# Kernel tuning notes

Measured on AMD Instinct MI355X. Metric: run time of the kernel, lower is better.

## Reference

```python
import jax, jax.numpy as jnp
import numpy as np

N = 8192
IN_F = 256
OUT_F = 64
ALPHA = 0.3  # LeakyReLU negative slope
NEG_INF = -9e15


def setup_inputs() -> dict:
    key = jax.random.key(0)
    k1, k2, k3, k4 = jax.random.split(key, 4)
    h = jax.random.normal(k1, (N, IN_F), dtype=jnp.float32)
    # sparse-ish binary adjacency with self loops (values are 0/1 floats)
    adj = (jax.random.uniform(k2, (N, N)) < 0.05).astype(jnp.float32)
    adj = jnp.maximum(adj, jnp.eye(N, dtype=jnp.float32))
    # xavier_uniform-style scales (gain=1.414)
    w_lim = 1.414 * np.sqrt(6.0 / (IN_F + OUT_F))
    a_lim = 1.414 * np.sqrt(6.0 / (2 * OUT_F + 1))
    W = jax.random.uniform(k3, (IN_F, OUT_F), minval=-w_lim, maxval=w_lim, dtype=jnp.float32)
    a = jax.random.uniform(k4, (2 * OUT_F, 1), minval=-a_lim, maxval=a_lim, dtype=jnp.float32)
    return {"h": h, "adj": adj, "W": W, "a": a}


def reference(h, adj, W, a):
    # Wh: [N, F]
    Wh = h @ W
    # Additive decomposition of the original concat-attention:
    # e_ij = leakyrelu(a[:F].Wh_i + a[F:].Wh_j)  -- identical math, no NxNx2F tensor
    src = Wh @ a[:OUT_F]      # [N, 1]
    dst = Wh @ a[OUT_F:]      # [N, 1]
    e = jax.nn.leaky_relu(src + dst.T, negative_slope=ALPHA)  # [N, N]
    e = e * adj               # faithful: original multiplies by adj before masking
    att = jnp.where(adj > 0, e, NEG_INF)
    att = jax.nn.softmax(att, axis=1)
    # dropout omitted (eval mode / deterministic reference)
    h_prime = att @ Wh        # [N, F]
    return jax.nn.elu(h_prime)
```

## Files before the change

kernel.cpp:

```cpp
#include <hip/hip_runtime.h>
#include <hip/hip_bf16.h>

#define N_NODES 8192
#define IN_F    256
#define OUT_F   64
#define ALPHA   0.3f
#define MBIAS   20.0f
#define CSPL    8
#define COLS_PER (N_NODES / CSPL)
#define NTILES  (COLS_PER / 64)
#define LDP     72
#define MROW    136
#define WH_BLOCKS (N_NODES / 16)

typedef unsigned short u16;
typedef unsigned int   u32;
typedef unsigned long long u64;
typedef __attribute__((ext_vector_type(8))) short bf16x8;
typedef __attribute__((ext_vector_type(4))) float f32x4;

__device__ __forceinline__ float bf2f(u32 u) { return __uint_as_float(u << 16); }
__device__ __forceinline__ u32 f2bfbits(float x) {
    u32 u = __float_as_uint(x);
    return (u + 0x7FFFu + ((u >> 16) & 1u)) >> 16;
}
__device__ __forceinline__ float lrelu(float s) { return s > 0.f ? s : ALPHA * s; }

__device__ __forceinline__ int detect_bf16(const void* adj) {
    return ((((const u32*)adj)[0] & 0xFFFFu) == 0x3F80u) ? 1 : 0;
}

template <bool BF16>
__device__ __forceinline__ float ld(const void* p, size_t idx) {
    if constexpr (BF16) return bf2f(((const u16*)p)[idx]);
    else                return ((const float*)p)[idx];
}

template <bool BF16>
__device__ __forceinline__ void wh4_impl(
    const void* __restrict__ h, const void* __restrict__ W,
    const void* __restrict__ a, float* __restrict__ src,
    float* __restrict__ dst, int i0, int lane, float* accv)
{
    float acc0 = 0.f, acc1 = 0.f, acc2 = 0.f, acc3 = 0.f;
#pragma unroll 8
    for (int k = 0; k < IN_F; ++k) {
        float wv = ld<BF16>(W, (size_t)k * OUT_F + lane);
        float h0 = ld<BF16>(h, (size_t)(i0 + 0) * IN_F + k);
        float h1 = ld<BF16>(h, (size_t)(i0 + 1) * IN_F + k);
        float h2 = ld<BF16>(h, (size_t)(i0 + 2) * IN_F + k);
        float h3 = ld<BF16>(h, (size_t)(i0 + 3) * IN_F + k);
        acc0 = fmaf(h0, wv, acc0);
        acc1 = fmaf(h1, wv, acc1);
        acc2 = fmaf(h2, wv, acc2);
        acc3 = fmaf(h3, wv, acc3);
    }
    float av = ld<BF16>(a, lane);
    float bv = ld<BF16>(a, OUT_F + lane);
    float accs[4] = {acc0, acc1, acc2, acc3};
#pragma unroll
    for (int r = 0; r < 4; ++r) {
        float ps = accs[r] * av, pd = accs[r] * bv;
#pragma unroll
        for (int off = 32; off > 0; off >>= 1) {
            ps += __shfl_xor(ps, off, 64);
            pd += __shfl_xor(pd, off, 64);
        }
        if (lane == 0) { src[i0 + r] = ps; dst[i0 + r] = pd; }
        accv[r] = accs[r];
    }
}

__global__ __launch_bounds__(256) void gat_prep_kernel(
    const void* __restrict__ h, const void* __restrict__ W,
    const void* __restrict__ a, const void* __restrict__ adj,
    u16* __restrict__ WhT, float* __restrict__ src, float* __restrict__ dst,
    u64* __restrict__ mask64)
{
    __shared__ float accs[16][OUT_F];
    const int tid = threadIdx.x, wave = tid >> 6, lane = tid & 63;
    const int isbf = detect_bf16(adj);

    if (blockIdx.x < WH_BLOCKS) {
        const int i0 = blockIdx.x * 16 + wave * 4;
        float av[4];
        if (isbf) wh4_impl<true >(h, W, a, src, dst, i0, lane, av);
        else      wh4_impl<false>(h, W, a, src, dst, i0, lane, av);
#pragma unroll
        for (int r = 0; r < 4; ++r) accs[wave * 4 + r][lane] = av[r];
        __syncthreads();
        if (tid < OUT_F) {
            u32 w[8];
#pragma unroll
            for (int e = 0; e < 8; ++e) {
                u32 lo = f2bfbits(accs[2 * e][tid]);
                u32 hi = f2bfbits(accs[2 * e + 1][tid]);
                w[e] = lo | (hi << 16);
            }
            u16* dstp = WhT + (size_t)tid * N_NODES + blockIdx.x * 16;
            *(uint4*)dstp       = *(uint4*)&w[0];
            *(uint4*)(dstp + 8) = *(uint4*)&w[4];
        }
    } else {
        const int wgid = (blockIdx.x - WH_BLOCKS) * 4 + wave;
        const int NW   = 2048 * 4;
        const int C    = (N_NODES / 256) * N_NODES;
        if (isbf) {
            const u16* base = (const u16*)adj;
            for (int c = wgid; c < C; c += NW) {
                const u16* p = base + (size_t)c * 256;
                u64 b0 = __ballot(p[lane]       != 0);
                u64 b1 = __ballot(p[64  + lane] != 0);
                u64 b2 = __ballot(p[128 + lane] != 0);
                u64 b3 = __ballot(p[192 + lane] != 0);
                u64 v = (lane == 0) ? b0 : (lane == 1) ? b1 : (lane == 2) ? b2 : b3;
                if (lane < 4) mask64[(size_t)c * 4 + lane] = v;
            }
        } else {
            const float* base = (const float*)adj;
            for (int c = wgid; c < C; c += NW) {
                const float* p = base + (size_t)c * 256;
                u64 b0 = __ballot(p[lane]       != 0.f);
                u64 b1 = __ballot(p[64  + lane] != 0.f);
                u64 b2 = __ballot(p[128 + lane] != 0.f);
                u64 b3 = __ballot(p[192 + lane] != 0.f);
                u64 v = (lane == 0) ? b0 : (lane == 1) ? b1 : (lane == 2) ? b2 : b3;
                if (lane < 4) mask64[(size_t)c * 4 + lane] = v;
            }
        }
    }
}

__global__ __launch_bounds__(256, 4) void gat_attn_kernel(
    const u64* __restrict__ mask64, const u16* __restrict__ WhT,
    const float* __restrict__ src, const float* __restrict__ dst,
    float* __restrict__ O_part, float* __restrict__ l_part)
{
    __shared__ alignas(16) u16 Plds[64 * LDP];
    __shared__ alignas(16) u16 Blds[64 * LDP];
    __shared__ alignas(16) unsigned char Mlds[64 * MROW];

    const int tid = threadIdx.x, wave = tid >> 6, lane = tid & 63;
    const int r = tid >> 2, cq = tid & 3;
    const int i0 = blockIdx.x * 64, c0 = blockIdx.y * COLS_PER;

    {
        const unsigned char* g = (const unsigned char*)mask64
            + (size_t)(i0 + r) * (N_NODES / 8) + (c0 >> 3) + cq * 32;
        *(uint4*)&Mlds[r * MROW + cq * 32]      = *(const uint4*)g;
        *(uint4*)&Mlds[r * MROW + cq * 32 + 16] = *(const uint4*)(g + 16);
    }

    const float srow = src[i0 + r];
    const float m = lrelu(srow + MBIAS);

    const u16*    whtrow = WhT + (size_t)r * N_NODES + c0 + cq * 16;
    const float4* dstp   = (const float4*)(dst + c0 + cq * 16);

    const int mrow = lane & 15, kq = (lane >> 4) * 8;

    f32x4 acc[4] = {{0,0,0,0},{0,0,0,0},{0,0,0,0},{0,0,0,0}};
    float lacc = 0.f;

    uint4 pb0 = *(const uint4*)(whtrow);
    uint4 pb1 = *(const uint4*)(whtrow + 8);

    __syncthreads();
    const u16* mrowp = (const u16*)&Mlds[r * MROW];

    for (int t = 0; t < NTILES; ++t) {
        *(uint4*)&Blds[r * LDP + cq * 16]     = pb0;
        *(uint4*)&Blds[r * LDP + cq * 16 + 8] = pb1;

        u32 msk = mrowp[t * 4 + cq];
        float4 d0 = dstp[t * 16],     d1 = dstp[t * 16 + 1];
        float4 d2 = dstp[t * 16 + 2], d3 = dstp[t * 16 + 3];
        float dv[16] = {d0.x,d0.y,d0.z,d0.w, d1.x,d1.y,d1.z,d1.w,
                        d2.x,d2.y,d2.z,d2.w, d3.x,d3.y,d3.z,d3.w};
        u32 po[8];
#pragma unroll
        for (int e = 0; e < 8; ++e) {
            float s0 = lrelu(srow + dv[2 * e]);
            float s1 = lrelu(srow + dv[2 * e + 1]);
            float p0 = (msk & (1u << (2 * e)))     ? __expf(s0 - m) : 0.f;
            float p1 = (msk & (1u << (2 * e + 1))) ? __expf(s1 - m) : 0.f;
            u32 q0 = f2bfbits(p0), q1 = f2bfbits(p1);
            lacc += bf2f(q0) + bf2f(q1);
            po[e] = q0 | (q1 << 16);
        }
        *(uint4*)&Plds[r * LDP + cq * 16]     = *(uint4*)&po[0];
        *(uint4*)&Plds[r * LDP + cq * 16 + 8] = *(uint4*)&po[4];

        __syncthreads();

        if (t + 1 < NTILES) {
            pb0 = *(const uint4*)(whtrow + (t + 1) * 64);
            pb1 = *(const uint4*)(whtrow + (t + 1) * 64 + 8);
        }

#pragma unroll
        for (int ks = 0; ks < 2; ++ks) {
            bf16x8 avf = *(bf16x8*)&Plds[(16 * wave + mrow) * LDP + ks * 32 + kq];
#pragma unroll
            for (int nt = 0; nt < 4; ++nt) {
                bf16x8 bvf = *(bf16x8*)&Blds[(16 * nt + mrow) * LDP + ks * 32 + kq];
                acc[nt] = __builtin_amdgcn_mfma_f32_16x16x32_bf16(avf, bvf, acc[nt], 0, 0, 0);
            }
        }
        __syncthreads();
    }

    lacc += __shfl_xor(lacc, 1, 64);
    lacc += __shfl_xor(lacc, 2, 64);
    if (cq == 0) l_part[blockIdx.y * N_NODES + i0 + r] = lacc;

    float* Ob = O_part + (size_t)blockIdx.y * N_NODES * OUT_F;
#pragma unroll
    for (int nt = 0; nt < 4; ++nt)
#pragma unroll
        for (int reg = 0; reg < 4; ++reg) {
            int row = i0 + 16 * wave + (lane >> 4) * 4 + reg;
            int col = 16 * nt + (lane & 15);
            Ob[(size_t)row * OUT_F + col] = acc[nt][reg];
        }
}

__global__ __launch_bounds__(256) void gat_reduce_kernel(
    const float* __restrict__ O_part, const float* __restrict__ l_part,
    const void* __restrict__ adj, void* __restrict__ out)
{
    int gid = blockIdx.x * 256 + threadIdx.x;
    int i = gid >> 6;
    float O = 0.f, L = 0.f;
#pragma unroll
    for (int c = 0; c < CSPL; ++c) {
        O += O_part[(size_t)c * N_NODES * OUT_F + gid];
        L += l_part[c * N_NODES + i];
    }
    float hp = O / L;
    float o = hp > 0.f ? hp : expm1f(hp);
    if (detect_bf16(adj)) ((u16*)out)[gid] = (u16)f2bfbits(o);
    else                  ((float*)out)[gid] = o;
}

extern "C" void kernel_launch(void* const* d_in, const int* in_sizes, int n_in,
                              void* d_out, int out_size, void* d_ws, size_t ws_size,
                              hipStream_t stream)
{
    const void* h   = d_in[0];
    const void* adj = d_in[1];
    const void* W   = d_in[2];
    const void* a   = d_in[3];

    char* ws = (char*)d_ws;
    u16*   WhT    = (u16*)ws;
    float* src    = (float*)(ws + (1u << 20));
    float* dst    = (float*)(ws + (1u << 20) + 32768);
    u64*   mask64 = (u64*)  (ws + (2u << 20));
    float* O_part = (float*)(ws + (16u << 20));
    float* l_part = (float*)(ws + (32u << 20));

    gat_prep_kernel<<<WH_BLOCKS + 2048, 256, 0, stream>>>(h, W, a, adj, WhT, src, dst, mask64);
    dim3 grid(N_NODES / 64, CSPL);
    gat_attn_kernel<<<grid, 256, 0, stream>>>(mask64, WhT, src, dst, O_part, l_part);
    gat_reduce_kernel<<<N_NODES * OUT_F / 256, 256, 0, stream>>>(O_part, l_part, adj, d_out);
}
```

Measured before the change: 426.8 us.

## Fuse adjacency bitmask construction into attention kernel, drop mask64 buffer

Removes the separate ballot pass that packed the dense adjacency into a global bitmask. Each attention thread now reads its own adjacency slice directly (up front, in chunks) and builds per-tile 16-bit masks in registers. This drops the write and re-read of the bitmask and the LDS staging with its barrier. In exchange the attention kernel issues large, strided, register-heavy loads of the full fp32 adjacency, which may raise register pressure and hurt occupancy under launch_bounds(256,4).

Result: slower. 455.5 us (+6.7%).

```diff
diff --git a/kernel.cpp b/kernel.cpp
--- a/kernel.cpp
+++ b/kernel.cpp
@@ -10,12 +10,9 @@
 #define COLS_PER (N_NODES / CSPL)
 #define NTILES  (COLS_PER / 64)
 #define LDP     72
-#define MROW    136
-#define WH_BLOCKS (N_NODES / 16)
 
 typedef unsigned short u16;
 typedef unsigned int   u32;
-typedef unsigned long long u64;
 typedef __attribute__((ext_vector_type(8))) short bf16x8;
 typedef __attribute__((ext_vector_type(4))) float f32x4;
 
@@ -71,84 +68,96 @@
     }
 }
 
-__global__ __launch_bounds__(256) void gat_prep_kernel(
+__global__ __launch_bounds__(256) void gat_wh_kernel(
     const void* __restrict__ h, const void* __restrict__ W,
     const void* __restrict__ a, const void* __restrict__ adj,
-    u16* __restrict__ WhT, float* __restrict__ src, float* __restrict__ dst,
-    u64* __restrict__ mask64)
+    u16* __restrict__ WhT, float* __restrict__ src, float* __restrict__ dst)
 {
     __shared__ float accs[16][OUT_F];
     const int tid = threadIdx.x, wave = tid >> 6, lane = tid & 63;
-    const int isbf = detect_bf16(adj);
-
-    if (blockIdx.x < WH_BLOCKS) {
-        const int i0 = blockIdx.x * 16 + wave * 4;
-        float av[4];
-        if (isbf) wh4_impl<true >(h, W, a, src, dst, i0, lane, av);
-        else      wh4_impl<false>(h, W, a, src, dst, i0, lane, av);
-#pragma unroll
-        for (int r = 0; r < 4; ++r) accs[wave * 4 + r][lane] = av[r];
-        __syncthreads();
-        if (tid < OUT_F) {
-            u32 w[8];
-#pragma unroll
-            for (int e = 0; e < 8; ++e) {
-                u32 lo = f2bfbits(accs[2 * e][tid]);
-                u32 hi = f2bfbits(accs[2 * e + 1][tid]);
-                w[e] = lo | (hi << 16);
-            }
-            u16* dstp = WhT + (size_t)tid * N_NODES + blockIdx.x * 16;
-            *(uint4*)dstp       = *(uint4*)&w[0];
-            *(uint4*)(dstp + 8) = *(uint4*)&w[4];
-        }
-    } else {
-        const int wgid = (blockIdx.x - WH_BLOCKS) * 4 + wave;
-        const int NW   = 2048 * 4;
-        const int C    = (N_NODES / 256) * N_NODES;
-        if (isbf) {
-            const u16* base = (const u16*)adj;
-            for (int c = wgid; c < C; c += NW) {
-                const u16* p = base + (size_t)c * 256;
-                u64 b0 = __ballot(p[lane]       != 0);
-                u64 b1 = __ballot(p[64  + lane] != 0);
-                u64 b2 = __ballot(p[128 + lane] != 0);
-                u64 b3 = __ballot(p[192 + lane] != 0);
-                u64 v = (lane == 0) ? b0 : (lane == 1) ? b1 : (lane == 2) ? b2 : b3;
-                if (lane < 4) mask64[(size_t)c * 4 + lane] = v;
-            }
-        } else {
-            const float* base = (const float*)adj;
-            for (int c = wgid; c < C; c += NW) {
-                const float* p = base + (size_t)c * 256;
-                u64 b0 = __ballot(p[lane]       != 0.f);
-                u64 b1 = __ballot(p[64  + lane] != 0.f);
-                u64 b2 = __ballot(p[128 + lane] != 0.f);
-                u64 b3 = __ballot(p[192 + lane] != 0.f);
-                u64 v = (lane == 0) ? b0 : (lane == 1) ? b1 : (lane == 2) ? b2 : b3;
-                if (lane < 4) mask64[(size_t)c * 4 + lane] = v;
-            }
-        }
+    const int i0 = blockIdx.x * 16 + wave * 4;
+    float av[4];
+    if (detect_bf16(adj)) wh4_impl<true >(h, W, a, src, dst, i0, lane, av);
+    else                  wh4_impl<false>(h, W, a, src, dst, i0, lane, av);
+#pragma unroll
+    for (int r = 0; r < 4; ++r) accs[wave * 4 + r][lane] = av[r];
+    __syncthreads();
+    if (tid < OUT_F) {
+        u32 w[8];
+#pragma unroll
+        for (int e = 0; e < 8; ++e) {
+            u32 lo = f2bfbits(accs[2 * e][tid]);
+            u32 hi = f2bfbits(accs[2 * e + 1][tid]);
+            w[e] = lo | (hi << 16);
+        }
+        u16* dstp = WhT + (size_t)tid * N_NODES + blockIdx.x * 16;
+        *(uint4*)dstp       = *(uint4*)&w[0];
+        *(uint4*)(dstp + 8) = *(uint4*)&w[4];
     }
 }
 
 __global__ __launch_bounds__(256, 4) void gat_attn_kernel(
-    const u64* __restrict__ mask64, const u16* __restrict__ WhT,
+    const void* __restrict__ adj, const u16* __restrict__ WhT,
     const float* __restrict__ src, const float* __restrict__ dst,
     float* __restrict__ O_part, float* __restrict__ l_part)
 {
     __shared__ alignas(16) u16 Plds[64 * LDP];
     __shared__ alignas(16) u16 Blds[64 * LDP];
-    __shared__ alignas(16) unsigned char Mlds[64 * MROW];
 
     const int tid = threadIdx.x, wave = tid >> 6, lane = tid & 63;
     const int r = tid >> 2, cq = tid & 3;
     const int i0 = blockIdx.x * 64, c0 = blockIdx.y * COLS_PER;
-
-    {
-        const unsigned char* g = (const unsigned char*)mask64
-            + (size_t)(i0 + r) * (N_NODES / 8) + (c0 >> 3) + cq * 32;
-        *(uint4*)&Mlds[r * MROW + cq * 32]      = *(const uint4*)g;
-        *(uint4*)&Mlds[r * MROW + cq * 32 + 16] = *(const uint4*)(g + 16);
+    const int isbf = detect_bf16(adj);
+
+    u32 mp[8] = {0, 0, 0, 0, 0, 0, 0, 0};
+    if (isbf) {
+        const u16* arow = (const u16*)adj + (size_t)(i0 + r) * N_NODES + c0 + cq * 16;
+#pragma unroll
+        for (int ch = 0; ch < 4; ++ch) {
+            uint4 v[8];
+#pragma unroll
+            for (int tt = 0; tt < 4; ++tt) {
+                v[2 * tt]     = *(const uint4*)(arow + (ch * 4 + tt) * 64);
+                v[2 * tt + 1] = *(const uint4*)(arow + (ch * 4 + tt) * 64 + 8);
+            }
+#pragma unroll
+            for (int tt = 0; tt < 4; ++tt) {
+                u32 ww[8] = {v[2*tt].x, v[2*tt].y, v[2*tt].z, v[2*tt].w,
+                             v[2*tt+1].x, v[2*tt+1].y, v[2*tt+1].z, v[2*tt+1].w};
+                u32 m16 = 0;
+#pragma unroll
+                for (int e = 0; e < 8; ++e) {
+                    if (ww[e] & 0xFFFFu) m16 |= 1u << (2 * e);
+                    if (ww[e] >> 16)     m16 |= 1u << (2 * e + 1);
+                }
+                int t = ch * 4 + tt;
+                mp[t >> 1] |= m16 << (16 * (t & 1));
+            }
+        }
+    } else {
+        const float* arow = (const float*)adj + (size_t)(i0 + r) * N_NODES + c0 + cq * 16;
+#pragma unroll
+        for (int ch = 0; ch < 4; ++ch) {
+            uint4 v[16];
+#pragma unroll
+            for (int tt = 0; tt < 4; ++tt)
+#pragma unroll
+                for (int q = 0; q < 4; ++q)
+                    v[4 * tt + q] = *(const uint4*)(arow + (ch * 4 + tt) * 64 + q * 4);
+#pragma unroll
+            for (int tt = 0; tt < 4; ++tt) {
+                u32 ww[16] = {v[4*tt].x,   v[4*tt].y,   v[4*tt].z,   v[4*tt].w,
+                              v[4*tt+1].x, v[4*tt+1].y, v[4*tt+1].z, v[4*tt+1].w,
+                              v[4*tt+2].x, v[4*tt+2].y, v[4*tt+2].z, v[4*tt+2].w,
+                              v[4*tt+3].x, v[4*tt+3].y, v[4*tt+3].z, v[4*tt+3].w};
+                u32 m16 = 0;
+#pragma unroll
+                for (int e = 0; e < 16; ++e)
+                    if (ww[e]) m16 |= 1u << e;
+                int t = ch * 4 + tt;
+                mp[t >> 1] |= m16 << (16 * (t & 1));
+            }
+        }
     }
 
     const float srow = src[i0 + r];
@@ -164,15 +173,12 @@
 
     uint4 pb0 = *(const uint4*)(whtrow);
     uint4 pb1 = *(const uint4*)(whtrow + 8);
-
-    __syncthreads();
-    const u16* mrowp = (const u16*)&Mlds[r * MROW];
 
     for (int t = 0; t < NTILES; ++t) {
         *(uint4*)&Blds[r * LDP + cq * 16]     = pb0;
         *(uint4*)&Blds[r * LDP + cq * 16 + 8] = pb1;
 
-        u32 msk = mrowp[t * 4 + cq];
+        u32 msk = (mp[t >> 1] >> (16 * (t & 1))) & 0xFFFFu;
         float4 d0 = dstp[t * 16],     d1 = dstp[t * 16 + 1];
         float4 d2 = dstp[t * 16 + 2], d3 = dstp[t * 16 + 3];
         float dv[16] = {d0.x,d0.y,d0.z,d0.w, d1.x,d1.y,d1.z,d1.w,
@@ -256,12 +262,11 @@
     u16*   WhT    = (u16*)ws;
     float* src    = (float*)(ws + (1u << 20));
     float* dst    = (float*)(ws + (1u << 20) + 32768);
-    u64*   mask64 = (u64*)  (ws + (2u << 20));
-    float* O_part = (float*)(ws + (16u << 20));
-    float* l_part = (float*)(ws + (32u << 20));
-
-    gat_prep_kernel<<<WH_BLOCKS + 2048, 256, 0, stream>>>(h, W, a, adj, WhT, src, dst, mask64);
+    float* O_part = (float*)(ws + (2u << 20));
+    float* l_part = (float*)(ws + (18u << 20));
+
+    gat_wh_kernel<<<N_NODES / 16, 256, 0, stream>>>(h, W, a, adj, WhT, src, dst);
     dim3 grid(N_NODES / 64, CSPL);
-    gat_attn_kernel<<<grid, 256, 0, stream>>>(mask64, WhT, src, dst, O_part, l_part);
+    gat_attn_kernel<<<grid, 256, 0, stream>>>(adj, WhT, src, dst, O_part, l_part);
     gat_reduce_kernel<<<N_NODES * OUT_F / 256, 256, 0, stream>>>(O_part, l_part, adj, d_out);
 }
```

## Fuse adjacency bitmask build into attention kernel and widen column split

Applied to the files above, without the earlier changes.

Removes the separate pass that packed the adjacency into a global bitmask and instead ballots the adjacency directly inside the attention kernel, writing per-block masks to LDS. The column split grows from 8 to 32, so each block handles 256 columns in a single stage. The whole WhT slice and the dst values are staged into LDS up front. Probabilities are computed straight into MFMA A-operand registers, which drops the P LDS round trip and the per-tile barriers. This saves one global write and read of the mask and many syncs, but partial-output traffic and the reduce work grow fourfold, and the adjacency read is no longer overlapped with the Wh computation.

After: 436.4 us. +2.3%, slower.

```diff
diff --git a/kernel.cpp b/kernel.cpp
--- a/kernel.cpp
+++ b/kernel.cpp
@@ -6,12 +6,9 @@
 #define OUT_F   64
 #define ALPHA   0.3f
 #define MBIAS   20.0f
-#define CSPL    8
+#define CSPL    32
 #define COLS_PER (N_NODES / CSPL)
-#define NTILES  (COLS_PER / 64)
-#define LDP     72
-#define MROW    136
-#define WH_BLOCKS (N_NODES / 16)
+#define BST     264
 
 typedef unsigned short u16;
 typedef unsigned int   u32;
@@ -71,148 +68,126 @@
     }
 }
 
-__global__ __launch_bounds__(256) void gat_prep_kernel(
+__global__ __launch_bounds__(256) void gat_wh_kernel(
     const void* __restrict__ h, const void* __restrict__ W,
     const void* __restrict__ a, const void* __restrict__ adj,
-    u16* __restrict__ WhT, float* __restrict__ src, float* __restrict__ dst,
-    u64* __restrict__ mask64)
+    u16* __restrict__ WhT, float* __restrict__ src, float* __restrict__ dst)
 {
     __shared__ float accs[16][OUT_F];
     const int tid = threadIdx.x, wave = tid >> 6, lane = tid & 63;
-    const int isbf = detect_bf16(adj);
-
-    if (blockIdx.x < WH_BLOCKS) {
-        const int i0 = blockIdx.x * 16 + wave * 4;
-        float av[4];
-        if (isbf) wh4_impl<true >(h, W, a, src, dst, i0, lane, av);
-        else      wh4_impl<false>(h, W, a, src, dst, i0, lane, av);
-#pragma unroll
-        for (int r = 0; r < 4; ++r) accs[wave * 4 + r][lane] = av[r];
-        __syncthreads();
-        if (tid < OUT_F) {
-            u32 w[8];
-#pragma unroll
-            for (int e = 0; e < 8; ++e) {
-                u32 lo = f2bfbits(accs[2 * e][tid]);
-                u32 hi = f2bfbits(accs[2 * e + 1][tid]);
-                w[e] = lo | (hi << 16);
-            }
-            u16* dstp = WhT + (size_t)tid * N_NODES + blockIdx.x * 16;
-            *(uint4*)dstp       = *(uint4*)&w[0];
-            *(uint4*)(dstp + 8) = *(uint4*)&w[4];
-        }
-    } else {
-        const int wgid = (blockIdx.x - WH_BLOCKS) * 4 + wave;
-        const int NW   = 2048 * 4;
-        const int C    = (N_NODES / 256) * N_NODES;
-        if (isbf) {
-            const u16* base = (const u16*)adj;
-            for (int c = wgid; c < C; c += NW) {
-                const u16* p = base + (size_t)c * 256;
-                u64 b0 = __ballot(p[lane]       != 0);
-                u64 b1 = __ballot(p[64  + lane] != 0);
-                u64 b2 = __ballot(p[128 + lane] != 0);
-                u64 b3 = __ballot(p[192 + lane] != 0);
-                u64 v = (lane == 0) ? b0 : (lane == 1) ? b1 : (lane == 2) ? b2 : b3;
-                if (lane < 4) mask64[(size_t)c * 4 + lane] = v;
-            }
-        } else {
-            const float* base = (const float*)adj;
-            for (int c = wgid; c < C; c += NW) {
-                const float* p = base + (size_t)c * 256;
-                u64 b0 = __ballot(p[lane]       != 0.f);
-                u64 b1 = __ballot(p[64  + lane] != 0.f);
-                u64 b2 = __ballot(p[128 + lane] != 0.f);
-                u64 b3 = __ballot(p[192 + lane] != 0.f);
-                u64 v = (lane == 0) ? b0 : (lane == 1) ? b1 : (lane == 2) ? b2 : b3;
-                if (lane < 4) mask64[(size_t)c * 4 + lane] = v;
-            }
-        }
+    const int i0 = blockIdx.x * 16 + wave * 4;
+    float av[4];
+    if (detect_bf16(adj)) wh4_impl<true >(h, W, a, src, dst, i0, lane, av);
+    else                  wh4_impl<false>(h, W, a, src, dst, i0, lane, av);
+#pragma unroll
+    for (int r = 0; r < 4; ++r) accs[wave * 4 + r][lane] = av[r];
+    __syncthreads();
+    if (tid < OUT_F) {
+        u32 w[8];
+#pragma unroll
+        for (int e = 0; e < 8; ++e) {
+            u32 lo = f2bfbits(accs[2 * e][tid]);
+            u32 hi = f2bfbits(accs[2 * e + 1][tid]);
+            w[e] = lo | (hi << 16);
+        }
+        u16* dstp = WhT + (size_t)tid * N_NODES + blockIdx.x * 16;
+        *(uint4*)dstp       = *(uint4*)&w[0];
+        *(uint4*)(dstp + 8) = *(uint4*)&w[4];
     }
 }
 
 __global__ __launch_bounds__(256, 4) void gat_attn_kernel(
-    const u64* __restrict__ mask64, const u16* __restrict__ WhT,
+    const void* __restrict__ adj, const u16* __restrict__ WhT,
     const float* __restrict__ src, const float* __restrict__ dst,
     float* __restrict__ O_part, float* __restrict__ l_part)
 {
-    __shared__ alignas(16) u16 Plds[64 * LDP];
-    __shared__ alignas(16) u16 Blds[64 * LDP];
-    __shared__ alignas(16) unsigned char Mlds[64 * MROW];
+    __shared__ alignas(16) u16  Blds[64 * BST];
+    __shared__ alignas(16) u64  Mlds[64 * 5];
+    __shared__ alignas(16) float Dlds[COLS_PER];
 
     const int tid = threadIdx.x, wave = tid >> 6, lane = tid & 63;
-    const int r = tid >> 2, cq = tid & 3;
     const int i0 = blockIdx.x * 64, c0 = blockIdx.y * COLS_PER;
+    const int isbf = detect_bf16(adj);
 
     {
-        const unsigned char* g = (const unsigned char*)mask64
-            + (size_t)(i0 + r) * (N_NODES / 8) + (c0 >> 3) + cq * 32;
-        *(uint4*)&Mlds[r * MROW + cq * 32]      = *(const uint4*)g;
-        *(uint4*)&Mlds[r * MROW + cq * 32 + 16] = *(const uint4*)(g + 16);
-    }
-
-    const float srow = src[i0 + r];
-    const float m = lrelu(srow + MBIAS);
-
-    const u16*    whtrow = WhT + (size_t)r * N_NODES + c0 + cq * 16;
-    const float4* dstp   = (const float4*)(dst + c0 + cq * 16);
+        const u16* wrow = WhT + (size_t)(tid >> 2) * N_NODES + c0 + (tid & 3) * 64;
+        u16* bl = &Blds[(tid >> 2) * BST + (tid & 3) * 64];
+#pragma unroll
+        for (int q = 0; q < 8; ++q)
+            *(uint4*)(bl + q * 8) = *(const uint4*)(wrow + q * 8);
+    }
+    Dlds[tid] = dst[c0 + tid];
+
+    if (isbf) {
+        const u16* base = (const u16*)adj;
+#pragma unroll 4
+        for (int rr = 0; rr < 16; ++rr) {
+            const int row = wave * 16 + rr;
+            const u16* p = base + (size_t)(i0 + row) * N_NODES + c0;
+            u64 b0 = __ballot(p[lane]       != 0);
+            u64 b1 = __ballot(p[64  + lane] != 0);
+            u64 b2 = __ballot(p[128 + lane] != 0);
+            u64 b3 = __ballot(p[192 + lane] != 0);
+            u64 v = (lane == 0) ? b0 : (lane == 1) ? b1 : (lane == 2) ? b2 : b3;
+            if (lane < 4) Mlds[row * 5 + lane] = v;
+        }
+    } else {
+        const float* base = (const float*)adj;
+#pragma unroll 4
+        for (int rr = 0; rr < 16; ++rr) {
+            const int row = wave * 16 + rr;
+            const float* p = base + (size_t)(i0 + row) * N_NODES + c0;
+            u64 b0 = __ballot(p[lane]       != 0.f);
+            u64 b1 = __ballot(p[64  + lane] != 0.f);
+            u64 b2 = __ballot(p[128 + lane] != 0.f);
+            u64 b3 = __ballot(p[192 + lane] != 0.f);
+            u64 v = (lane == 0) ? b0 : (lane == 1) ? b1 : (lane == 2) ? b2 : b3;
+            if (lane < 4) Mlds[row * 5 + lane] = v;
+        }
+    }
+
+    __syncthreads();
 
     const int mrow = lane & 15, kq = (lane >> 4) * 8;
+    const int mloc = 16 * wave + mrow;
+    const float srow = src[i0 + mloc];
+    const float mbound = lrelu(srow + MBIAS);
 
     f32x4 acc[4] = {{0,0,0,0},{0,0,0,0},{0,0,0,0},{0,0,0,0}};
     float lacc = 0.f;
 
-    uint4 pb0 = *(const uint4*)(whtrow);
-    uint4 pb1 = *(const uint4*)(whtrow + 8);
-
-    __syncthreads();
-    const u16* mrowp = (const u16*)&Mlds[r * MROW];
-
-    for (int t = 0; t < NTILES; ++t) {
-        *(uint4*)&Blds[r * LDP + cq * 16]     = pb0;
-        *(uint4*)&Blds[r * LDP + cq * 16 + 8] = pb1;
-
-        u32 msk = mrowp[t * 4 + cq];
-        float4 d0 = dstp[t * 16],     d1 = dstp[t * 16 + 1];
-        float4 d2 = dstp[t * 16 + 2], d3 = dstp[t * 16 + 3];
-        float dv[16] = {d0.x,d0.y,d0.z,d0.w, d1.x,d1.y,d1.z,d1.w,
-                        d2.x,d2.y,d2.z,d2.w, d3.x,d3.y,d3.z,d3.w};
-        u32 po[8];
-#pragma unroll
-        for (int e = 0; e < 8; ++e) {
-            float s0 = lrelu(srow + dv[2 * e]);
-            float s1 = lrelu(srow + dv[2 * e + 1]);
-            float p0 = (msk & (1u << (2 * e)))     ? __expf(s0 - m) : 0.f;
-            float p1 = (msk & (1u << (2 * e + 1))) ? __expf(s1 - m) : 0.f;
-            u32 q0 = f2bfbits(p0), q1 = f2bfbits(p1);
-            lacc += bf2f(q0) + bf2f(q1);
-            po[e] = q0 | (q1 << 16);
-        }
-        *(uint4*)&Plds[r * LDP + cq * 16]     = *(uint4*)&po[0];
-        *(uint4*)&Plds[r * LDP + cq * 16 + 8] = *(uint4*)&po[4];
-
-        __syncthreads();
-
-        if (t + 1 < NTILES) {
-            pb0 = *(const uint4*)(whtrow + (t + 1) * 64);
-            pb1 = *(const uint4*)(whtrow + (t + 1) * 64 + 8);
-        }
-
+#pragma unroll
+    for (int t = 0; t < 4; ++t) {
+        const u64 mword = Mlds[mloc * 5 + t];
 #pragma unroll
         for (int ks = 0; ks < 2; ++ks) {
-            bf16x8 avf = *(bf16x8*)&Plds[(16 * wave + mrow) * LDP + ks * 32 + kq];
+            const u32 bits = (u32)(mword >> (ks * 32 + kq)) & 0xFFu;
+            const float* dp = &Dlds[t * 64 + ks * 32 + kq];
+            float4 dd0 = *(const float4*)dp;
+            float4 dd1 = *(const float4*)(dp + 4);
+            float dv[8] = {dd0.x,dd0.y,dd0.z,dd0.w, dd1.x,dd1.y,dd1.z,dd1.w};
+            union { u32 w[4]; bf16x8 v; } pa;
+#pragma unroll
+            for (int e = 0; e < 4; ++e) {
+                float s0 = lrelu(srow + dv[2 * e]);
+                float s1 = lrelu(srow + dv[2 * e + 1]);
+                float p0 = (bits & (1u << (2 * e)))     ? __expf(s0 - mbound) : 0.f;
+                float p1 = (bits & (1u << (2 * e + 1))) ? __expf(s1 - mbound) : 0.f;
+                u32 q0 = f2bfbits(p0), q1 = f2bfbits(p1);
+                lacc += bf2f(q0) + bf2f(q1);
+                pa.w[e] = q0 | (q1 << 16);
+            }
 #pragma unroll
             for (int nt = 0; nt < 4; ++nt) {
-                bf16x8 bvf = *(bf16x8*)&Blds[(16 * nt + mrow) * LDP + ks * 32 + kq];
-                acc[nt] = __builtin_amdgcn_mfma_f32_16x16x32_bf16(avf, bvf, acc[nt], 0, 0, 0);
+                bf16x8 bvf = *(bf16x8*)&Blds[(16 * nt + mrow) * BST + t * 64 + ks * 32 + kq];
+                acc[nt] = __builtin_amdgcn_mfma_f32_16x16x32_bf16(pa.v, bvf, acc[nt], 0, 0, 0);
             }
         }
-        __syncthreads();
-    }
-
-    lacc += __shfl_xor(lacc, 1, 64);
-    lacc += __shfl_xor(lacc, 2, 64);
-    if (cq == 0) l_part[blockIdx.y * N_NODES + i0 + r] = lacc;
+    }
+
+    lacc += __shfl_xor(lacc, 16, 64);
+    lacc += __shfl_xor(lacc, 32, 64);
+    if (lane < 16) l_part[blockIdx.y * N_NODES + i0 + 16 * wave + lane] = lacc;
 
     float* Ob = O_part + (size_t)blockIdx.y * N_NODES * OUT_F;
 #pragma unroll
@@ -232,7 +207,7 @@
     int gid = blockIdx.x * 256 + threadIdx.x;
     int i = gid >> 6;
     float O = 0.f, L = 0.f;
-#pragma unroll
+#pragma unroll 8
     for (int c = 0; c < CSPL; ++c) {
         O += O_part[(size_t)c * N_NODES * OUT_F + gid];
         L += l_part[c * N_NODES + i];
@@ -256,12 +231,11 @@
     u16*   WhT    = (u16*)ws;
     float* src    = (float*)(ws + (1u << 20));
     float* dst    = (float*)(ws + (1u << 20) + 32768);
-    u64*   mask64 = (u64*)  (ws + (2u << 20));
-    float* O_part = (float*)(ws + (16u << 20));
-    float* l_part = (float*)(ws + (32u << 20));
-
-    gat_prep_kernel<<<WH_BLOCKS + 2048, 256, 0, stream>>>(h, W, a, adj, WhT, src, dst, mask64);
+    float* O_part = (float*)(ws + (2u << 20));
+    float* l_part = (float*)(ws + (66u << 20));
+
+    gat_wh_kernel<<<N_NODES / 16, 256, 0, stream>>>(h, W, a, adj, WhT, src, dst);
     dim3 grid(N_NODES / 64, CSPL);
-    gat_attn_kernel<<<grid, 256, 0, stream>>>(mask64, WhT, src, dst, O_part, l_part);
+    gat_attn_kernel<<<grid, 256, 0, stream>>>(adj, WhT, src, dst, O_part, l_part);
     gat_reduce_kernel<<<N_NODES * OUT_F / 256, 256, 0, stream>>>(O_part, l_part, adj, d_out);
 }
```
